# Kernel optimization log

Measured on AMD Instinct MI355X. Metric: run time of the kernel, lower is better.

The kernel has to match this reference:

```python
import jax, jax.numpy as jnp
import numpy as np

DEPTH, DIM, DH, H, DQ, V = 4, 1024, 4096, 8, 128, 32000
B, L = 2, 1024


def setup_inputs() -> dict:
    key = jax.random.key(0)
    ks = iter(jax.random.split(key, 48))
    def nrm(shape, scale=1.0):
        return jax.random.normal(next(ks), shape, jnp.float32) * scale
    d = {}
    d["x"] = nrm((B, L, V))
    d["tin_w"] = nrm((DIM, V), V ** -0.5)
    d["tin_b"] = nrm((DIM,), 0.02)
    d["tout_w"] = nrm((V, DIM), DIM ** -0.5)
    d["tout_b"] = nrm((V,), 0.02)
    d["wq_w"] = nrm((DEPTH, H * DQ, DIM), DIM ** -0.5)
    d["wq_b"] = nrm((DEPTH, H * DQ), 0.02)
    d["wk_w"] = nrm((DEPTH, H * DQ, DIM), DIM ** -0.5)
    d["wk_b"] = nrm((DEPTH, H * DQ), 0.02)
    d["wv_w"] = nrm((DEPTH, H * DQ, DIM), DIM ** -0.5)
    d["wv_b"] = nrm((DEPTH, H * DQ), 0.02)
    d["wo_w"] = nrm((DEPTH, DIM, H * DQ), (H * DQ) ** -0.5)
    d["wo_b"] = nrm((DEPTH, DIM), 0.02)
    d["f1_w"] = nrm((DEPTH, DH, DIM), DIM ** -0.5)
    d["f1_b"] = nrm((DEPTH, DH), 0.02)
    d["f2_w"] = nrm((DEPTH, DIM, DH), DH ** -0.5)
    d["f2_b"] = nrm((DEPTH, DIM), 0.02)
    d["phz_re"] = nrm((DEPTH, H, DQ))
    d["phz_im"] = nrm((DEPTH, H, DQ))
    d["amp"] = nrm((DEPTH, H))
    d["lc_re"] = nrm((DEPTH, H, DQ, DQ), 0.02)
    d["lc_im"] = nrm((DEPTH, H, DQ, DQ), 0.02)
    return d


def _layernorm(x):
    m = x.mean(-1, keepdims=True)
    v = ((x - m) ** 2).mean(-1, keepdims=True)
    return (x - m) * jax.lax.rsqrt(v + 1e-5)


def _retention(x, qw, qb, kw, kb, vw, vb, ow, ob, pre, pim, amp, lcr, lci):
    b, l, _ = x.shape
    q = (x @ qw.T + qb).reshape(b, l, H, DQ)
    k = (x @ kw.T + kb).reshape(b, l, H, DQ)
    v = (x @ vw.T + vb).reshape(b, l, H, DQ)
    pz = pre + 1j * pim                              # [H,DQ] complex
    phase = pz / jnp.abs(pz)                         # unit modulus
    a = jax.nn.sigmoid(amp)                          # [H]
    phazor = phase * a[:, None]
    n = jnp.arange(l)
    pp = phase[None, :, :] ** n[:, None, None]       # [L,H,DQ]
    pp_inv = phase[None, :, :] ** (-n)[:, None, None]
    php = phazor[None, :, :] ** n[:, None, None]
    lc = jax.lax.stop_gradient(lcr + 1j * lci)       # [H,DQ,DQ], detached in torch
    qc = q.astype(jnp.complex64)
    kc = k.astype(jnp.complex64)
    vc = v.astype(jnp.complex64)
    cross = jnp.einsum('blhd,lhd,hde->blhe', qc, php * phazor[None], lc)
    tril = n[:, None] >= n[None, :]
    expn = jnp.where(tril, n[:, None] - n[None, :], 0)           # [L,L]
    mask = jnp.where(tril[None], a[:, None, None] ** expn[None], 0.0)  # [H,L,L]
    qk = jnp.einsum('blhd,bmhd->bhlm', qc * pp[None], kc * pp_inv[None])
    inner = jnp.einsum('bhlm,bmhd->blhd', qk * mask[None].astype(jnp.complex64), vc)
    y = jax.nn.silu((inner + cross).real).reshape(b, l, H * DQ)
    return y @ ow.T + ob


def reference(x, tin_w, tin_b, tout_w, tout_b, wq_w, wq_b, wk_w, wk_b, wv_w, wv_b,
              wo_w, wo_b, f1_w, f1_b, f2_w, f2_b, phz_re, phz_im, amp, lc_re, lc_im):
    h = x @ tin_w.T + tin_b
    for i in range(DEPTH):
        r = _retention(_layernorm(h), wq_w[i], wq_b[i], wk_w[i], wk_b[i],
                       wv_w[i], wv_b[i], wo_w[i], wo_b[i],
                       phz_re[i], phz_im[i], amp[i], lc_re[i], lc_im[i])
        h = h + r
        f = _layernorm(h)
        f = jax.nn.silu(f @ f1_w[i].T + f1_b[i]) @ f2_w[i].T + f2_b[i]
        h = h + f
    return h @ tout_w.T + tout_b
```

## Files before the change

### kernel.cpp

```cpp
#include <hip/hip_runtime.h>
#include <hip/hip_bf16.h>
#include <stdint.h>

#define DEPTH 4
#define DIM   1024
#define DH    4096
#define NH    8
#define DQ    128
#define VOC   32000
#define BATCH 2
#define SEQ   1024
#define ROWS  (BATCH*SEQ)
#define CROSSK 256
#define LDS_X (CROSSK + SEQ)

#define PQKV  ((long long)ROWS*DIM)
#define PQKV3 ((long long)ROWS*3*DIM)
#define PROT  ((long long)BATCH*NH*SEQ*2*DQ)
#define PMID  ((long long)ROWS*DH)
#define PY    ((long long)ROWS*DIM)

typedef __hip_bfloat16 bf16;
using f32x4  = __attribute__((ext_vector_type(4))) float;
using bf16x8 = __attribute__((ext_vector_type(8))) __bf16;

__device__ __forceinline__ unsigned short bcu(bf16 h) {
  return __builtin_bit_cast(unsigned short, h);
}

__device__ __forceinline__ void wpair(bf16* p, long long off, long long plane, float v) {
  bf16 hi = __float2bfloat16(v);
  p[off] = hi;
  p[off + plane] = __float2bfloat16(v - __bfloat162float(hi));
}

__device__ __forceinline__ void gload_lds16(const void* g, void* l) {
  __builtin_amdgcn_global_load_lds(
      (const __attribute__((address_space(1))) void*)g,
      (__attribute__((address_space(3))) void*)(uintptr_t)l,
      16, 0, 0);
}

#define BM 128
#define BN 128
#define BKK 64
#define PL 16384

template<int EPI, int SA, int SB>
__global__ __launch_bounds__(256, (SA || SB) ? 2 : 4)
void gemm_bt(const bf16* __restrict__ A, long long sA, long long pA, int lda,
             const bf16* __restrict__ B, long long sB, long long pB, int ldb, int bmod,
             void* __restrict__ Cv, long long sC, long long pC, int ldc,
             const float* __restrict__ bias, int hmod,
             int M, int N, int K, int ksplit, int causal)
{
  __shared__ int4 sbuf[1024 * (2 + SA + SB)];
  char* Asb = (char*)sbuf;
  char* Bsb = Asb + PL * (1 + SA);

  const int tid  = threadIdx.x;
  const int lane = tid & 63;
  const int wave = tid >> 6;
  const int wr   = wave >> 1;
  const int wc   = wave & 1;
  const int z    = blockIdx.z;
  const int zb   = z / ksplit;
  const int ks   = z - zb * ksplit;
  const int Kc   = K / ksplit;
  const int k0   = ks * Kc;
  const int tm   = blockIdx.x * BM;
  const int tn   = blockIdx.y * BN;

  if (causal == 1 && tn >= tm + BM) return;
  int kend = k0 + Kc;
  if (causal == 2) {
    kend = min(kend, tm + BM + CROSSK);
    if (kend <= k0) return;
  }

  const bf16* Ab = A + (long long)zb * sA;
  const bf16* Bb = B + (long long)(zb % bmod) * sB;

  f32x4 acc[4][4] = {};

  for (int kt = k0; kt < kend; kt += BKK) {
#pragma unroll
    for (int j = 0; j < 4; ++j) {
      int slot0 = j*256 + wave*64;
      int i = slot0 + lane;
      int row = i >> 3;
      int gc  = (i & 7) ^ (row & 7);
      long long ga = (long long)(tm + row) * lda + kt + gc*8;
      long long gb = (long long)(tn + row) * ldb + kt + gc*8;
      gload_lds16(Ab + ga, Asb + slot0*16);
      if (SA) gload_lds16(Ab + pA + ga, Asb + PL + slot0*16);
      gload_lds16(Bb + gb, Bsb + slot0*16);
      if (SB) gload_lds16(Bb + pB + gb, Bsb + PL + slot0*16);
    }
    __syncthreads();
#pragma unroll
    for (int kh = 0; kh < 2; ++kh) {
      const int cb = kh*4 + (lane >> 4);
      int4 avh[4], bvh[4], avl[4], bvl[4];
#pragma unroll
      for (int mi = 0; mi < 4; ++mi) {
        int m = wr*64 + mi*16 + (lane & 15);
        int off = m*128 + ((cb ^ (m & 7)) << 4);
        avh[mi] = *(const int4*)(Asb + off);
        if (SA) avl[mi] = *(const int4*)(Asb + PL + off);
      }
#pragma unroll
      for (int nj = 0; nj < 4; ++nj) {
        int n = wc*64 + nj*16 + (lane & 15);
        int off = n*128 + ((cb ^ (n & 7)) << 4);
        bvh[nj] = *(const int4*)(Bsb + off);
        if (SB) bvl[nj] = *(const int4*)(Bsb + PL + off);
      }
#pragma unroll
      for (int mi = 0; mi < 4; ++mi)
#pragma unroll
        for (int nj = 0; nj < 4; ++nj)
          acc[mi][nj] = __builtin_amdgcn_mfma_f32_16x16x32_bf16(
              __builtin_bit_cast(bf16x8, avh[mi]),
              __builtin_bit_cast(bf16x8, bvh[nj]), acc[mi][nj], 0, 0, 0);
      if (SA)
#pragma unroll
        for (int mi = 0; mi < 4; ++mi)
#pragma unroll
          for (int nj = 0; nj < 4; ++nj)
            acc[mi][nj] = __builtin_amdgcn_mfma_f32_16x16x32_bf16(
                __builtin_bit_cast(bf16x8, avl[mi]),
                __builtin_bit_cast(bf16x8, bvh[nj]), acc[mi][nj], 0, 0, 0);
      if (SB)
#pragma unroll
        for (int mi = 0; mi < 4; ++mi)
#pragma unroll
          for (int nj = 0; nj < 4; ++nj)
            acc[mi][nj] = __builtin_amdgcn_mfma_f32_16x16x32_bf16(
                __builtin_bit_cast(bf16x8, avh[mi]),
                __builtin_bit_cast(bf16x8, bvl[nj]), acc[mi][nj], 0, 0, 0);
    }
    __syncthreads();
  }

  const float* dtab = (EPI == 7) ? bias + (zb % hmod) * (SEQ + 1) : nullptr;
  const int col = lane & 15;
  const int rb  = (lane >> 4) << 2;
  float* Cf = (float*)Cv + (long long)zb * sC;
  bf16*  Ch = (bf16*) Cv + (long long)zb * sC;

#pragma unroll
  for (int mi = 0; mi < 4; ++mi)
#pragma unroll
    for (int nj = 0; nj < 4; ++nj) {
      long long gn = tn + wc*64 + nj*16 + col;
      float bv_ = (EPI != 7 && bias && ks == 0) ? bias[gn] : 0.f;
#pragma unroll
      for (int r = 0; r < 4; ++r) {
        long long gm = tm + wr*64 + mi*16 + rb + r;
        float v = acc[mi][nj][r] + bv_;
        long long off = gm * (long long)ldc + gn;
        if (EPI == 0)      Cf[off] = v;
        else if (EPI == 3) { if (ksplit > 1) atomicAdd(&Cf[off], v); else Cf[off] += v; }
        else if (EPI == 5) wpair(Ch, off, pC, v);
        else if (EPI == 6) wpair(Ch, off, pC, v / (1.f + __expf(-v)));
        else {
          long long dlt = gm - gn;
          float dcy = (dlt >= 0) ? dtab[dlt] : 0.f;
          Ch[off] = __float2bfloat16(acc[mi][nj][r] * dcy);
        }
      }
    }
}

#define MC_LC (NH*DQ*DQ)
#define MC_TH (MC_LC + NH*DQ)
#define MC_B3 (MC_TH + 3*DIM)
#define MC_DC (MC_B3 + NH*(SEQ+1))
#define MC_ZR (MC_DC + (BATCH*NH*SEQ*DQ)/4)
__global__ void prep_kernel(const float* __restrict__ wq, const float* __restrict__ wk,
                            const float* __restrict__ wv, const float* __restrict__ wo,
                            const float* __restrict__ f1, const float* __restrict__ f2,
                            bf16* __restrict__ Wqkv, bf16* __restrict__ Wol,
                            bf16* __restrict__ Wf1, bf16* __restrict__ Wf2,
                            const float* __restrict__ lcr, const float* __restrict__ lci,
                            bf16* __restrict__ vte,
                            const float* __restrict__ pre, const float* __restrict__ pim,
                            float* __restrict__ theta,
                            const float* __restrict__ bq, const float* __restrict__ bk,
                            const float* __restrict__ bv, float* __restrict__ qkvbi,
                            const float* __restrict__ amp, float* __restrict__ dtab,
                            float4* __restrict__ retz) {
  const long long S1 = (long long)DIM*DIM;
  const long long S4 = S1 >> 2;
  const long long WPq = 3*S1;
  const long long CW4 = 12*S4;
  long long i = (long long)blockIdx.x * blockDim.x + threadIdx.x;
  if (i < CW4) {
    const float* src; bf16 *hi, *lo; long long j4;
    if (i < 3*S4) {
      int t = (int)(i / S4);
      src = (t == 0) ? wq : (t == 1) ? wk : wv;
      j4 = i - (long long)t * S4;
      hi = Wqkv + (long long)t * S1; lo = hi + WPq;
    } else if (i < 4*S4)  { src = wo; j4 = i - 3*S4; hi = Wol; lo = Wol + S1; }
    else if (i < 8*S4)    { src = f1; j4 = i - 4*S4; hi = Wf1; lo = Wf1 + 4*S1; }
    else                  { src = f2; j4 = i - 8*S4; hi = Wf2; lo = nullptr; }
    float4 v = ((const float4*)src)[j4];
    bf16 h0 = __float2bfloat16(v.x), h1 = __float2bfloat16(v.y);
    bf16 h2 = __float2bfloat16(v.z), h3 = __float2bfloat16(v.w);
    ((ushort4*)hi)[j4] = ushort4{bcu(h0), bcu(h1), bcu(h2), bcu(h3)};
    if (lo) {
      bf16 l0 = __float2bfloat16(v.x - __bfloat162float(h0));
      bf16 l1 = __float2bfloat16(v.y - __bfloat162float(h1));
      bf16 l2 = __float2bfloat16(v.z - __bfloat162float(h2));
      bf16 l3 = __float2bfloat16(v.w - __bfloat162float(h3));
      ((ushort4*)lo)[j4] = ushort4{bcu(l0), bcu(l1), bcu(l2), bcu(l3)};
    }
    return;
  }
  long long j = i - CW4;
  if (j < MC_LC) {
    int d = (int)(j & 127), e = (int)((j >> 7) & 127), h = (int)(j >> 14);
    float vr = lcr[((long long)h*DQ + d)*DQ + e];
    float vi = lci[((long long)h*DQ + d)*DQ + e];
    bf16 br = __float2bfloat16(vr), bi = __float2bfloat16(-vi);
#pragma unroll
    for (int b = 0; b < BATCH; ++b) {
      long long base = ((long long)(b*NH + h)*DQ + e) * LDS_X;
      vte[base + d]      = br;
      vte[base + DQ + d] = bi;
    }
  } else if (j < MC_TH) {
    int t = (int)(j - MC_LC);
    theta[t] = atan2f(pim[t], pre[t]);
  } else if (j < MC_B3) {
    int t = (int)(j - MC_TH);
    qkvbi[t] = (t < DIM) ? bq[t] : (t < 2*DIM) ? bk[t - DIM] : bv[t - 2*DIM];
  } else if (j < MC_DC) {
    int t = (int)(j - MC_B3);
    int h = t / (SEQ+1), n = t % (SEQ+1);
    float a = 1.f / (1.f + __expf(-amp[h]));
    dtab[t] = powf(a, (float)n);
  } else if (j < MC_ZR) {
    retz[j - MC_DC] = float4{0.f, 0.f, 0.f, 0.f};
  }
}

#define TIN_X4 ((long long)ROWS*VOC/4)
#define TIN_W4 (TIN_X4 + (long long)DIM*VOC/4)
#define TIN_H4 (TIN_W4 + (long long)ROWS*DIM/4)
__global__ void tinprep_kernel(const float* __restrict__ x, bf16* __restrict__ xb,
                               const float* __restrict__ tw, bf16* __restrict__ twb,
                               float4* __restrict__ hz) {
  long long i = (long long)blockIdx.x * blockDim.x + threadIdx.x;
  const float* src; bf16* dst; long long j;
  if (i < TIN_X4)      { src = x;  dst = xb;  j = i; }
  else if (i < TIN_W4) { src = tw; dst = twb; j = i - TIN_X4; }
  else if (i < TIN_H4) { hz[i - TIN_W4] = float4{0.f,0.f,0.f,0.f}; return; }
  else return;
  float4 v = ((const float4*)src)[j];
  ushort4 o{bcu(__float2bfloat16(v.x)), bcu(__float2bfloat16(v.y)),
            bcu(__float2bfloat16(v.z)), bcu(__float2bfloat16(v.w))};
  ((ushort4*)dst)[j] = o;
}

#define TAIL_H (PQKV)
#define TAIL_W (TAIL_H + (long long)VOC*DIM/4)
__global__ void tailprep_kernel(const float* __restrict__ h, bf16* __restrict__ hb,
                                const float* __restrict__ tw, bf16* __restrict__ twb) {
  long long i = (long long)blockIdx.x * blockDim.x + threadIdx.x;
  if (i < TAIL_H) {
    float v = h[i];
    bf16 hi = __float2bfloat16(v);
    hb[i] = hi;
    hb[i + PQKV] = __float2bfloat16(v - __bfloat162float(hi));
  } else if (i < TAIL_W) {
    long long j = i - TAIL_H;
    float4 v = ((const float4*)tw)[j];
    ushort4 o{bcu(__float2bfloat16(v.x)), bcu(__float2bfloat16(v.y)),
              bcu(__float2bfloat16(v.z)), bcu(__float2bfloat16(v.w))};
    ((ushort4*)twb)[j] = o;
  }
}

__global__ void ln_kernel(const float* __restrict__ in, bf16* __restrict__ out) {
  const int row = blockIdx.x;
  const int tid = threadIdx.x;
  const float4 v = ((const float4*)(in + (size_t)row*DIM))[tid];
  float s  = v.x + v.y + v.z + v.w;
  float s2 = v.x*v.x + v.y*v.y + v.z*v.z + v.w*v.w;
#pragma unroll
  for (int o = 32; o > 0; o >>= 1) { s += __shfl_xor(s, o); s2 += __shfl_xor(s2, o); }
  __shared__ float red[8];
  const int wv = tid >> 6;
  if ((tid & 63) == 0) { red[wv] = s; red[4 + wv] = s2; }
  __syncthreads();
  s  = red[0] + red[1] + red[2] + red[3];
  s2 = red[4] + red[5] + red[6] + red[7];
  const float mean = s * (1.f / DIM);
  const float var  = s2 * (1.f / DIM) - mean * mean;
  const float inv  = rsqrtf(var + 1e-5f);
  float e0 = (v.x - mean) * inv, e1 = (v.y - mean) * inv;
  float e2 = (v.z - mean) * inv, e3 = (v.w - mean) * inv;
  bf16 h0 = __float2bfloat16(e0), h1 = __float2bfloat16(e1);
  bf16 h2 = __float2bfloat16(e2), h3 = __float2bfloat16(e3);
  bf16 l0 = __float2bfloat16(e0 - __bfloat162float(h0));
  bf16 l1 = __float2bfloat16(e1 - __bfloat162float(h1));
  bf16 l2 = __float2bfloat16(e2 - __bfloat162float(h2));
  bf16 l3 = __float2bfloat16(e3 - __bfloat162float(h3));
  ((ushort4*)(out + (size_t)row*DIM))[tid]        = ushort4{bcu(h0), bcu(h1), bcu(h2), bcu(h3)};
  ((ushort4*)(out + PQKV + (size_t)row*DIM))[tid] = ushort4{bcu(l0), bcu(l1), bcu(l2), bcu(l3)};
}

__global__ void rotate_kernel(const bf16* __restrict__ qkv,
                              const float* __restrict__ theta_t,
                              const float* __restrict__ dtab,
                              bf16* __restrict__ qrot, bf16* __restrict__ krot,
                              bf16* __restrict__ SbX) {
  const int d = threadIdx.x, l = blockIdx.x, h = blockIdx.y, b = blockIdx.z;
  const float theta = theta_t[h*DQ + d];
  const long long rowb = (long long)(b*SEQ + l)*(3*DIM) + h*DQ + d;
  const float qv = __bfloat162float(qkv[rowb]) + __bfloat162float(qkv[rowb + PQKV3]);
  const float kv = __bfloat162float(qkv[rowb + DIM]) + __bfloat162float(qkv[rowb + DIM + PQKV3]);
  float sn, cs;
  sincosf(theta * (float)l, &sn, &cs);
  const long long dst = ((long long)(b*NH + h)*SEQ + l)*(2*DQ) + d;
  qrot[dst]      = __float2bfloat16(qv * cs);
  qrot[dst + DQ] = __float2bfloat16(qv * sn);
  krot[dst]      = __float2bfloat16(kv * cs);
  krot[dst + DQ] = __float2bfloat16(kv * sn);
  float sn2, cs2;
  sincosf(theta * (float)(l + 1), &sn2, &cs2);
  const float ad = dtab[h*(SEQ+1) + l + 1];
  const long long qw = ((long long)(b*NH + h)*SEQ + l)*LDS_X + d;
  SbX[qw]      = __float2bfloat16(qv * ad * cs2);
  SbX[qw + DQ] = __float2bfloat16(qv * ad * sn2);
}

__global__ void vt_kernel(const bf16* __restrict__ qkv, bf16* __restrict__ vte) {
  __shared__ float tile[64][65];
  const int t  = threadIdx.x;
  const int c  = t & 63, r4 = t >> 6;
  const int m0 = blockIdx.x * 64;
  const int d0 = blockIdx.y * 64;
  const int h  = blockIdx.z & (NH - 1);
  const int b  = blockIdx.z >> 3;
#pragma unroll
  for (int rr = 0; rr < 64; rr += 4) {
    const int m = m0 + rr + r4;
    const long long src = (long long)(b*SEQ + m)*(3*DIM) + 2*DIM + h*DQ + d0 + c;
    tile[rr + r4][c] = __bfloat162float(qkv[src]) + __bfloat162float(qkv[src + PQKV3]);
  }
  __syncthreads();
#pragma unroll
  for (int rr = 0; rr < 64; rr += 4) {
    const int d = rr + r4;
    vte[((long long)(b*NH + h)*DQ + d0 + d)*LDS_X + CROSSK + m0 + c] =
        __float2bfloat16(tile[c][d]);
  }
}

__global__ void siluret_kernel(const float* __restrict__ ret, bf16* __restrict__ y) {
  const int d = threadIdx.x, l = blockIdx.x, h = blockIdx.y, b = blockIdx.z;
  float r = ret[((long long)(b*NH + h)*SEQ + l)*DQ + d];
  float s = r / (1.f + __expf(-r));
  wpair(y, ((long long)(b*SEQ + l)*NH + h)*DQ + d, PY, s);
}

extern "C" void kernel_launch(void* const* d_in, const int* in_sizes, int n_in,
                              void* d_out, int out_size, void* d_ws, size_t ws_size,
                              hipStream_t stream) {
  const float* x      = (const float*)d_in[0];
  const float* tin_w  = (const float*)d_in[1];
  const float* tin_b  = (const float*)d_in[2];
  const float* tout_w = (const float*)d_in[3];
  const float* tout_b = (const float*)d_in[4];
  const float* wq_w   = (const float*)d_in[5];
  const float* wq_b   = (const float*)d_in[6];
  const float* wk_w   = (const float*)d_in[7];
  const float* wk_b   = (const float*)d_in[8];
  const float* wv_w   = (const float*)d_in[9];
  const float* wv_b   = (const float*)d_in[10];
  const float* wo_w   = (const float*)d_in[11];
  const float* wo_b   = (const float*)d_in[12];
  const float* f1_w   = (const float*)d_in[13];
  const float* f1_b   = (const float*)d_in[14];
  const float* f2_w   = (const float*)d_in[15];
  const float* f2_b   = (const float*)d_in[16];
  const float* phz_re = (const float*)d_in[17];
  const float* phz_im = (const float*)d_in[18];
  const float* amp    = (const float*)d_in[19];
  const float* lc_re  = (const float*)d_in[20];
  const float* lc_im  = (const float*)d_in[21];
  (void)in_sizes; (void)n_in; (void)out_size; (void)ws_size;

  char* w = (char*)d_ws;
  auto alloc = [&](size_t bytes) {
    char* p = w; w += (bytes + 255) & ~(size_t)255; return p;
  };
  auto palloc = [&](long long elems) {
    return (bf16*)alloc((size_t)elems * 2 * 2);
  };

  const long long WP = 3LL*DIM*DIM;
  float* h     = (float*)alloc((size_t)ROWS*DIM*4);
  float* ret   = (float*)alloc((size_t)BATCH*NH*SEQ*DQ*4);
  float* qkvbi = (float*)alloc((size_t)3*DIM*4);
  float* dtab  = (float*)alloc((size_t)NH*(SEQ+1)*4);
  float* theta = (float*)alloc((size_t)NH*DQ*4);
  bf16*  hb    = palloc(PQKV);
  bf16*  Wqkv  = palloc(WP);
  bf16*  Wol   = palloc((long long)DIM*DIM);
  bf16*  Wf1l  = palloc((long long)DH*DIM);
  bf16*  Wf2l  = (bf16*)alloc((size_t)DIM*DH*2);
  bf16*  qkvb  = palloc(PQKV3);
  bf16*  Wbig  = (bf16*)alloc((size_t)DIM*VOC*2);
  bf16*  qrot  = (bf16*)alloc((size_t)PROT*2);
  bf16*  krot  = (bf16*)alloc((size_t)PROT*2);
  bf16*  SbX   = (bf16*)alloc((size_t)BATCH*NH*SEQ*LDS_X*2);
  bf16*  vte   = (bf16*)alloc((size_t)BATCH*NH*DQ*LDS_X*2);
  bf16*  mid   = palloc(PMID);
  bf16*  xb = (bf16*)d_out;
  bf16*  yb = qkvb;

  auto gemm = [&](int epi, int sa, int sb, const bf16* A, long long sA, long long pA, int lda,
                  const bf16* B, long long sB, long long pB, int ldb, int bmod,
                  void* C, long long sC, long long pC, int ldc,
                  const float* bias, int hmod, int M, int N, int K, int batch,
                  int ksplit, int causal) {
    dim3 g(M / BM, N / BN, batch * ksplit), blk(256);
    if (epi == 3 && !sa && !sb)      gemm_bt<3,0,0><<<g, blk, 0, stream>>>(A,sA,pA,lda,B,sB,pB,ldb,bmod,C,sC,pC,ldc,bias,hmod,M,N,K,ksplit,causal);
    else if (epi == 7)               gemm_bt<7,0,0><<<g, blk, 0, stream>>>(A,sA,pA,lda,B,sB,pB,ldb,bmod,C,sC,pC,ldc,bias,hmod,M,N,K,ksplit,causal);
    else if (epi == 0 && sa && !sb)  gemm_bt<0,1,0><<<g, blk, 0, stream>>>(A,sA,pA,lda,B,sB,pB,ldb,bmod,C,sC,pC,ldc,bias,hmod,M,N,K,ksplit,causal);
    else if (epi == 3 && sa && !sb)  gemm_bt<3,1,0><<<g, blk, 0, stream>>>(A,sA,pA,lda,B,sB,pB,ldb,bmod,C,sC,pC,ldc,bias,hmod,M,N,K,ksplit,causal);
    else if (epi == 3)               gemm_bt<3,1,1><<<g, blk, 0, stream>>>(A,sA,pA,lda,B,sB,pB,ldb,bmod,C,sC,pC,ldc,bias,hmod,M,N,K,ksplit,causal);
    else if (epi == 5)               gemm_bt<5,1,1><<<g, blk, 0, stream>>>(A,sA,pA,lda,B,sB,pB,ldb,bmod,C,sC,pC,ldc,bias,hmod,M,N,K,ksplit,causal);
    else if (epi == 6)               gemm_bt<6,1,1><<<g, blk, 0, stream>>>(A,sA,pA,lda,B,sB,pB,ldb,bmod,C,sC,pC,ldc,bias,hmod,M,N,K,ksplit,causal);
  };
  const int BIG = 1 << 30;

  tinprep_kernel<<<dim3((unsigned)((TIN_H4 + 255) / 256)), dim3(256), 0, stream>>>(
      x, xb, tin_w, Wbig, (float4*)h);
  gemm(3, 0, 0, xb, 0, 0, VOC, Wbig, 0, 0, VOC, BIG, h, 0, 0, DIM, tin_b, 1,
       ROWS, DIM, VOC, 1, 10, 0);

  for (int i = 0; i < DEPTH; ++i) {
    {
      long long tot = 12LL*((long long)DIM*DIM >> 2) + MC_ZR;
      prep_kernel<<<dim3((unsigned)((tot + 255) / 256)), dim3(256), 0, stream>>>(
          wq_w + (size_t)i*DIM*DIM, wk_w + (size_t)i*DIM*DIM, wv_w + (size_t)i*DIM*DIM,
          wo_w + (size_t)i*DIM*DIM, f1_w + (size_t)i*DH*DIM, f2_w + (size_t)i*DIM*DH,
          Wqkv, Wol, Wf1l, Wf2l,
          lc_re + (size_t)i*NH*DQ*DQ, lc_im + (size_t)i*NH*DQ*DQ, vte,
          phz_re + i*NH*DQ, phz_im + i*NH*DQ, theta,
          wq_b + i*DIM, wk_b + i*DIM, wv_b + i*DIM, qkvbi,
          amp + i*NH, dtab, (float4*)ret);
    }

    ln_kernel<<<ROWS, 256, 0, stream>>>(h, hb);
    gemm(5, 1, 1, hb, 0, PQKV, DIM, Wqkv, 0, WP, DIM, BIG,
         qkvb, 0, PQKV3, 3*DIM, qkvbi, 1, ROWS, 3*DIM, DIM, 1, 1, 0);
    rotate_kernel<<<dim3(SEQ, NH, BATCH), DQ, 0, stream>>>(
        qkvb, theta, dtab, qrot, krot, SbX);
    vt_kernel<<<dim3(SEQ/64, DQ/64, BATCH*NH), 256, 0, stream>>>(qkvb, vte);
    gemm(7, 0, 0, qrot, (long long)SEQ*2*DQ, 0, 2*DQ,
         krot, (long long)SEQ*2*DQ, 0, 2*DQ, BIG,
         SbX + CROSSK, (long long)SEQ*LDS_X, 0, LDS_X, dtab, NH,
         SEQ, SEQ, 2*DQ, BATCH*NH, 1, 1);
    gemm(3, 0, 0, SbX, (long long)SEQ*LDS_X, 0, LDS_X,
         vte, (long long)DQ*LDS_X, 0, LDS_X, BIG,
         ret, (long long)SEQ*DQ, 0, DQ, nullptr, 1, SEQ, DQ, LDS_X, BATCH*NH, 4, 2);
    siluret_kernel<<<dim3(SEQ, NH, BATCH), DQ, 0, stream>>>(ret, yb);
    gemm(3, 1, 1, yb, 0, PY, DIM, Wol, 0, (long long)DIM*DIM, DIM, BIG,
         h, 0, 0, DIM, wo_b + i*DIM, 1, ROWS, DIM, DIM, 1, 2, 0);

    ln_kernel<<<ROWS, 256, 0, stream>>>(h, hb);
    gemm(6, 1, 1, hb, 0, PQKV, DIM, Wf1l, 0, (long long)DH*DIM, DIM, BIG,
         mid, 0, PMID, DH, f1_b + i*DH, 1, ROWS, DH, DIM, 1, 1, 0);
    gemm(3, 1, 0, mid, 0, PMID, DH, Wf2l, 0, 0, DH, BIG,
         h, 0, 0, DIM, f2_b + i*DIM, 1, ROWS, DIM, DH, 1, 4, 0);
  }

  tailprep_kernel<<<dim3((unsigned)((TAIL_W + 255) / 256)), dim3(256), 0, stream>>>(
      h, hb, tout_w, Wbig);
  gemm(0, 1, 0, hb, 0, PQKV, DIM, Wbig, 0, 0, DIM, BIG,
       (float*)d_out, 0, 0, VOC, tout_b, 1, ROWS, VOC, DIM, 1, 1, 0);
}
```

Measured before the change: 1.739 ms.

## Use 256x256-tile pipelined MFMA GEMM for output projection

Adds a new 512-thread GEMM kernel with 256x256 tiles, double-buffered direct-to-LDS loads, XOR-swizzled LDS, explicit waitcnt scheduling and XCD-aware block remapping. It replaces the generic 128x128 gemm_bt path for the large vocabulary output projection (2048x32000x1024, split-bf16 two-pass A). Larger tiles raise arithmetic intensity and the interleaved loads aim to overlap memory with MFMA work, at the cost of heavy LDS use (128KB) and lower occupancy. The remap assumes the block count divides by 8, which holds here (8x125=1000 blocks).

```diff
diff --git a/kernel.cpp b/kernel.cpp
--- a/kernel.cpp
+++ b/kernel.cpp
@@ -39,6 +39,136 @@
       (const __attribute__((address_space(1))) void*)g,
       (__attribute__((address_space(3))) void*)(uintptr_t)l,
       16, 0, 0);
+}
+
+#define VMW(n) asm volatile("s_waitcnt vmcnt(" #n ")" ::: "memory")
+
+__device__ __forceinline__ int2 xcd_remap(int gx, int gy) {
+  int f   = blockIdx.x + gx * blockIdx.y;
+  int nwg = gx * gy;
+  int fp  = (f & 7) * (nwg >> 3) + (f >> 3);
+  return int2{fp % gx, fp / gx};
+}
+
+template<int NPASS>
+__global__ __launch_bounds__(512, 2)
+void gemm256(const bf16* __restrict__ A, long long aoff1, int lda,
+             const bf16* __restrict__ B, long long boff1, int ldb,
+             float* __restrict__ C, int ldc,
+             const float* __restrict__ bias,
+             int M, int N, int K)
+{
+  __shared__ char sh[131072];
+  const int tid  = threadIdx.x;
+  const int lane = tid & 63;
+  const int wid  = tid >> 6;
+  const int wr   = wid >> 2;
+  const int wc   = wid & 3;
+  const int2 xy  = xcd_remap(gridDim.x, gridDim.y);
+  const int tm   = xy.x * 256;
+  const int tn   = xy.y * 256;
+  const int nt   = K * NPASS / 64;
+
+  auto stage = [&](int g, int u) {
+    const int b = g & 1;
+    int kt = g * 64;
+    long long ao = 0, bo = 0;
+    if (NPASS == 2 && kt >= K) { ao = aoff1; bo = boff1; kt -= K; }
+    const int isB  = (u < 2);
+    const int half = u & 1;
+#pragma unroll
+    for (int ld = 0; ld < 2; ++ld) {
+      int row = half*128 + ld*64 + (tid >> 3);
+      int gc  = (tid & 7) ^ (row & 7);
+      const bf16* src = isB
+          ? (B + bo + (long long)(tn + row) * ldb + kt + gc*8)
+          : (A + ao + (long long)(tm + row) * lda + kt + gc*8);
+      gload_lds16(src, sh + b*65536 + (isB ? 32768 : 0) + half*16384
+                        + ld*8192 + wid*1024);
+    }
+  };
+  auto rdA = [&](int b, int mf, int ks) -> int4 {
+    int m = wr*128 + mf*16 + (lane & 15);
+    int c = ks*4 + (lane >> 4);
+    return *(const int4*)(sh + b*65536 + m*128 + ((c ^ (m & 7)) << 4));
+  };
+  auto rdB = [&](int b, int g, int ks) -> int4 {
+    int n = wc*64 + g*16 + (lane & 15);
+    int c = ks*4 + (lane >> 4);
+    return *(const int4*)(sh + b*65536 + 32768 + n*128 + ((c ^ (n & 7)) << 4));
+  };
+
+  f32x4 acc[8][4] = {};
+  int4  bfr[2][4];
+
+  stage(0,0); stage(0,1); stage(0,2); stage(0,3);
+  if (nt > 1) { stage(1,0); stage(1,1); VMW(4); } else { VMW(0); }
+  __builtin_amdgcn_s_barrier();
+  __builtin_amdgcn_sched_barrier(0);
+
+  for (int j = 0; j < nt; ++j) {
+    const int b = j & 1;
+#pragma unroll
+    for (int q = 0; q < 4; ++q) {
+      const int mf0 = 2*q, mf1 = 2*q + 1;
+      int4 a0 = rdA(b, mf0, 0), a1 = rdA(b, mf0, 1);
+      int4 a2 = rdA(b, mf1, 0), a3 = rdA(b, mf1, 1);
+      if (q == 0) {
+#pragma unroll
+        for (int ks = 0; ks < 2; ++ks)
+#pragma unroll
+          for (int g = 0; g < 4; ++g) bfr[ks][g] = rdB(b, g, ks);
+      }
+      if (q == 0 && j+1 < nt) stage(j+1, 2);
+      if (q == 1 && j+1 < nt) stage(j+1, 3);
+      if (q == 2 && j+2 < nt) stage(j+2, 0);
+      if (q == 3 && j+2 < nt) stage(j+2, 1);
+      __builtin_amdgcn_s_barrier();
+      asm volatile("s_waitcnt lgkmcnt(0)" ::: "memory");
+      __builtin_amdgcn_sched_barrier(0);
+      __builtin_amdgcn_s_setprio(1);
+#pragma unroll
+      for (int g = 0; g < 4; ++g)
+        acc[mf0][g] = __builtin_amdgcn_mfma_f32_16x16x32_bf16(
+            __builtin_bit_cast(bf16x8, a0), __builtin_bit_cast(bf16x8, bfr[0][g]),
+            acc[mf0][g], 0, 0, 0);
+#pragma unroll
+      for (int g = 0; g < 4; ++g)
+        acc[mf0][g] = __builtin_amdgcn_mfma_f32_16x16x32_bf16(
+            __builtin_bit_cast(bf16x8, a1), __builtin_bit_cast(bf16x8, bfr[1][g]),
+            acc[mf0][g], 0, 0, 0);
+#pragma unroll
+      for (int g = 0; g < 4; ++g)
+        acc[mf1][g] = __builtin_amdgcn_mfma_f32_16x16x32_bf16(
+            __builtin_bit_cast(bf16x8, a2), __builtin_bit_cast(bf16x8, bfr[0][g]),
+            acc[mf1][g], 0, 0, 0);
+#pragma unroll
+      for (int g = 0; g < 4; ++g)
+        acc[mf1][g] = __builtin_amdgcn_mfma_f32_16x16x32_bf16(
+            __builtin_bit_cast(bf16x8, a3), __builtin_bit_cast(bf16x8, bfr[1][g]),
+            acc[mf1][g], 0, 0, 0);
+      __builtin_amdgcn_s_setprio(0);
+      if (q == 1) { if (j+1 < nt) VMW(8); else VMW(0); }
+      if (q == 3) { if (j+2 < nt) VMW(5); else if (j+1 < nt) VMW(1); }
+      __builtin_amdgcn_s_barrier();
+      __builtin_amdgcn_sched_barrier(0);
+    }
+  }
+
+  const int col = lane & 15;
+  const int rb  = (lane >> 4) << 2;
+#pragma unroll
+  for (int mf = 0; mf < 8; ++mf)
+#pragma unroll
+    for (int g = 0; g < 4; ++g) {
+      long long gn = tn + wc*64 + g*16 + col;
+      float bv = bias ? bias[gn] : 0.f;
+#pragma unroll
+      for (int r = 0; r < 4; ++r) {
+        long long gm = tm + wr*128 + mf*16 + rb + r;
+        C[gm * (long long)ldc + gn] = acc[mf][g][r] + bv;
+      }
+    }
 }
 
 #define BM 128
@@ -432,7 +562,6 @@
     dim3 g(M / BM, N / BN, batch * ksplit), blk(256);
     if (epi == 3 && !sa && !sb)      gemm_bt<3,0,0><<<g, blk, 0, stream>>>(A,sA,pA,lda,B,sB,pB,ldb,bmod,C,sC,pC,ldc,bias,hmod,M,N,K,ksplit,causal);
     else if (epi == 7)               gemm_bt<7,0,0><<<g, blk, 0, stream>>>(A,sA,pA,lda,B,sB,pB,ldb,bmod,C,sC,pC,ldc,bias,hmod,M,N,K,ksplit,causal);
-    else if (epi == 0 && sa && !sb)  gemm_bt<0,1,0><<<g, blk, 0, stream>>>(A,sA,pA,lda,B,sB,pB,ldb,bmod,C,sC,pC,ldc,bias,hmod,M,N,K,ksplit,causal);
     else if (epi == 3 && sa && !sb)  gemm_bt<3,1,0><<<g, blk, 0, stream>>>(A,sA,pA,lda,B,sB,pB,ldb,bmod,C,sC,pC,ldc,bias,hmod,M,N,K,ksplit,causal);
     else if (epi == 3)               gemm_bt<3,1,1><<<g, blk, 0, stream>>>(A,sA,pA,lda,B,sB,pB,ldb,bmod,C,sC,pC,ldc,bias,hmod,M,N,K,ksplit,causal);
     else if (epi == 5)               gemm_bt<5,1,1><<<g, blk, 0, stream>>>(A,sA,pA,lda,B,sB,pB,ldb,bmod,C,sC,pC,ldc,bias,hmod,M,N,K,ksplit,causal);
@@ -484,6 +613,6 @@
 
   tailprep_kernel<<<dim3((unsigned)((TAIL_W + 255) / 256)), dim3(256), 0, stream>>>(
       h, hb, tout_w, Wbig);
-  gemm(0, 1, 0, hb, 0, PQKV, DIM, Wbig, 0, 0, DIM, BIG,
-       (float*)d_out, 0, 0, VOC, tout_b, 1, ROWS, VOC, DIM, 1, 1, 0);
-}
+  gemm256<2><<<dim3(ROWS/256, VOC/256, 1), dim3(512), 0, stream>>>(
+      hb, PQKV, DIM, Wbig, 0, DIM, (float*)d_out, VOC, tout_b, ROWS, VOC, DIM);
+}
```

Result: slower. 1.779 ms (+2.3%).
